# Kernel tuning notes

Hardware: AMD Instinct MI355X
Metric: run time of the kernel (lower is better)

The kernel has to match this reference:

```python
import jax, jax.numpy as jnp
import numpy as np

NUM_SEQS = 4
SEQ_LEN = 2048
T = NUM_SEQS * SEQ_LEN          # total tokens
D_IN = 4096
D_OUT = 4096
NUM_ADAPTERS = 8
MAX_RANK = 64
CACHE_LEN = NUM_ADAPTERS * MAX_RANK  # 512 pages


def setup_inputs() -> dict:
    key = jax.random.key(0)
    ks = jax.random.split(key, 8)
    x = jax.random.normal(ks[0], (T, D_IN), dtype=jnp.float32)
    weight = jax.random.normal(ks[1], (D_OUT, D_IN), dtype=jnp.float32) * 0.02
    bias = jax.random.normal(ks[2], (D_OUT,), dtype=jnp.float32) * 0.02
    a_cache = jax.random.normal(ks[3], (CACHE_LEN, D_IN), dtype=jnp.float32) * 0.02
    b_cache = jax.random.normal(ks[4], (CACHE_LEN, D_OUT), dtype=jnp.float32) * 0.02
    b_start_loc = (jnp.arange(NUM_SEQS) * SEQ_LEN).astype(jnp.int32)
    b_adapter_ids = jax.random.randint(ks[5], (NUM_SEQS,), 0, NUM_ADAPTERS).astype(jnp.int32)
    b_scaling = jax.random.uniform(ks[6], (NUM_SEQS,), dtype=jnp.float32, minval=0.5, maxval=2.0)
    # page i for (adapter a, rank slot r) lives at a*MAX_RANK + r
    rank_page_table = jnp.arange(CACHE_LEN, dtype=jnp.int32).reshape(NUM_ADAPTERS, MAX_RANK)
    ranks = jax.random.randint(ks[7], (NUM_ADAPTERS,), 1, MAX_RANK + 1).astype(jnp.int32)
    return {"x": x, "weight": weight, "bias": bias, "a_cache": a_cache,
            "b_cache": b_cache, "b_start_loc": b_start_loc,
            "b_adapter_ids": b_adapter_ids, "b_scaling": b_scaling,
            "rank_page_table": rank_page_table, "ranks": ranks}


def reference(x, weight, bias, a_cache, b_cache, b_start_loc,
              b_adapter_ids, b_scaling, rank_page_table, ranks):
    t = x.shape[0]
    num_adapters, max_rank = rank_page_table.shape
    # map each token to its sequence -> adapter id / scaling (mbgmm dispatch)
    seg = jnp.searchsorted(b_start_loc, jnp.arange(t, dtype=b_start_loc.dtype),
                           side='right') - 1                      # [T]
    tok_adapter = b_adapter_ids[seg]                              # [T]
    tok_scale = b_scaling[seg]                                    # [T]
    # gather paged LoRA A/B weights per adapter: [A, R, D]
    A_all = a_cache[rank_page_table]                              # [A, R, D_in]
    B_all = b_cache[rank_page_table]                              # [A, R, D_out]
    # mbgmm_a: xa[t, r] = x[t] . A[adapter(t), r], zero beyond rank
    xa_all = jnp.einsum('td,ard->tar', x, A_all)                  # [T, A, R]
    rmask = (jnp.arange(max_rank)[None, :] < ranks[:, None])      # [A, R]
    onehot = (tok_adapter[:, None] == jnp.arange(num_adapters)[None, :])  # [T, A]
    sel = (onehot[:, :, None] & rmask[None, :, :]).astype(x.dtype)  # [T, A, R]
    xa_sel = xa_all * sel
    # mbgmm_b: lora_out[t] = scaling * sum_r xa[t, r] * B[adapter(t), r]
    lora_out = jnp.einsum('tar,aro->to', xa_sel, B_all) * tok_scale[:, None]
    base_out = x @ weight.T + bias
    return base_out + lora_out
```

## Files before the change

### kernel.cpp

```cpp
#include <hip/hip_runtime.h>
#include <hip/hip_bf16.h>

typedef unsigned short u16;
typedef unsigned int u32;
typedef __attribute__((ext_vector_type(8))) short bf16x8;
typedef __attribute__((ext_vector_type(4))) float f32x4;

#define T_TOK 8192
#define DIN 4096
#define DOUT 4096
#define N_SEQS 4
#define N_ADPT 8
#define MAXR 64
#define CACHE_LEN 512

__device__ __forceinline__ u16 f2bf(float f) {
    u32 u = __builtin_bit_cast(u32, f);
    u += 0x7fffu + ((u >> 16) & 1u);
    return (u16)(u >> 16);
}

__device__ __forceinline__ void load_lds16(const u16* g, u16* l) {
    __builtin_amdgcn_global_load_lds(
        (const __attribute__((address_space(1))) u32*)g,
        (__attribute__((address_space(3))) u32*)l, 16, 0, 0);
}

__global__ void cvt_kernel(const float* __restrict__ in, u16* __restrict__ out, int n4) {
    int i = blockIdx.x * blockDim.x + threadIdx.x;
    int stride = gridDim.x * blockDim.x;
    for (; i < n4; i += stride) {
        float4 v = reinterpret_cast<const float4*>(in)[i];
        ushort4 o;
        o.x = f2bf(v.x); o.y = f2bf(v.y); o.z = f2bf(v.z); o.w = f2bf(v.w);
        reinterpret_cast<ushort4*>(out)[i] = o;
    }
}

__global__ void build_bt(const float* __restrict__ b_cache, const int* __restrict__ rpt,
                         u16* __restrict__ Bt) {
    int id = blockIdx.x * 256 + threadIdx.x;
    int n  = id & (DOUT - 1);
    int rb = (id >> 12) & 7;
    int a  = id >> 15;
    union { u16 u[8]; uint4 v; } pack;
    #pragma unroll
    for (int j = 0; j < 8; ++j) {
        int r = rb * 8 + j;
        int page = rpt[a * MAXR + r];
        pack.u[j] = f2bf(b_cache[(long)page * DOUT + n]);
    }
    *reinterpret_cast<uint4*>(&Bt[((long)(a * DOUT + n)) * MAXR + rb * 8]) = pack.v;
}

__launch_bounds__(256)
__global__ void xa_kernel(const u16* __restrict__ xb, const u16* __restrict__ ab,
                          const int* __restrict__ b_start_loc,
                          const int* __restrict__ b_adapter_ids,
                          const float* __restrict__ b_scaling,
                          const int* __restrict__ rpt,
                          const int* __restrict__ ranks,
                          u16* __restrict__ xa) {
    int t0 = blockIdx.x * 128;
    int seg = 0;
    #pragma unroll
    for (int i = 1; i < N_SEQS; ++i) if (b_start_loc[i] <= t0) seg = i;
    int adapter = b_adapter_ids[seg];
    float scale = b_scaling[seg];
    int rank = ranks[adapter];

    __shared__ __attribute__((aligned(16))) u16 As[128 * 32];
    __shared__ __attribute__((aligned(16))) u16 Bs[64 * 32];

    int tid = threadIdx.x;
    int lane = tid & 63, wave = tid >> 6;
    int lr = lane & 15, lk = lane >> 4;

    int e0 = wave * 64 + lane;
    int e1 = 256 + e0;
    int ra0 = e0 >> 2, ca0 = (e0 & 3) * 8;
    int ra1 = e1 >> 2, ca1 = (e1 & 3) * 8;
    const u16* gA0 = xb + (long)(t0 + ra0) * DIN + ca0;
    const u16* gA1 = xb + (long)(t0 + ra1) * DIN + ca1;
    int rB = ra0;
    int page = rpt[adapter * MAXR + rB];
    const u16* gB = ab + (long)page * DIN + ca0;

    f32x4 acc[2][4] = {};

    for (int k0 = 0; k0 < DIN; k0 += 32) {
        load_lds16(gA0 + k0, As + wave * 512);
        load_lds16(gA1 + k0, As + 2048 + wave * 512);
        load_lds16(gB + k0,  Bs + wave * 512);
        asm volatile("s_waitcnt vmcnt(0)" ::: "memory");
        __syncthreads();
        bf16x8 af[2], bfr[4];
        #pragma unroll
        for (int m = 0; m < 2; ++m)
            af[m] = *(const bf16x8*)&As[(wave * 32 + m * 16 + lr) * 32 + lk * 8];
        #pragma unroll
        for (int n = 0; n < 4; ++n)
            bfr[n] = *(const bf16x8*)&Bs[(n * 16 + lr) * 32 + lk * 8];
        #pragma unroll
        for (int m = 0; m < 2; ++m)
            #pragma unroll
            for (int n = 0; n < 4; ++n)
                acc[m][n] = __builtin_amdgcn_mfma_f32_16x16x32_bf16(af[m], bfr[n], acc[m][n], 0, 0, 0);
        __syncthreads();
    }

    #pragma unroll
    for (int m = 0; m < 2; ++m) {
        int trow = t0 + wave * 32 + m * 16 + lk * 4;
        #pragma unroll
        for (int n = 0; n < 4; ++n) {
            int r = n * 16 + lr;
            #pragma unroll
            for (int j = 0; j < 4; ++j) {
                float v = (r < rank) ? acc[m][n][j] * scale : 0.0f;
                xa[(long)(trow + j) * MAXR + r] = f2bf(v);
            }
        }
    }
}

__launch_bounds__(512, 2)
__global__ void gemm256_kernel(const u16* __restrict__ xb, const u16* __restrict__ wb,
                               const float* __restrict__ bias,
                               const u16* __restrict__ xa, const u16* __restrict__ Bt,
                               const int* __restrict__ b_start_loc,
                               const int* __restrict__ b_adapter_ids,
                               float* __restrict__ out) {
    __shared__ __attribute__((aligned(16))) u16 lds[65536];

    int bid = blockIdx.x;
    int wgid = (bid & 7) * 64 + (bid >> 3);
    int mt = wgid >> 4, nt = wgid & 15;
    int brow = mt * 256, bcol = nt * 256;

    int seg = 0;
    #pragma unroll
    for (int i = 1; i < N_SEQS; ++i) if (b_start_loc[i] <= brow) seg = i;
    int adapter = b_adapter_ids[seg];

    int tid = threadIdx.x;
    int lane = tid & 63, wave = tid >> 6;
    int wm = wave >> 2, wn = wave & 3;
    int lr = lane & 15, lk = lane >> 4;

    int rb = tid >> 3;
    int cs = (tid & 7) ^ (rb & 7);
    const u16* aSrc  = xb + (long)(brow + rb) * DIN + cs * 8;
    const u16* wSrc  = wb + (long)(bcol + rb) * DIN + cs * 8;
    const u16* xaSrc = xa + (long)(brow + rb) * MAXR + cs * 8;
    const u16* btSrc = Bt + ((long)(adapter * DOUT + bcol + rb)) * MAXR + cs * 8;

    f32x4 acc[8][4] = {};

    #define STAGE(srcA, ldA, srcB, ldB, buf)                                        \
        do {                                                                        \
            u16* al = lds + (buf) * 16384 + wave * 512;                             \
            u16* bl = lds + 32768 + (buf) * 16384 + wave * 512;                     \
            _Pragma("unroll")                                                       \
            for (int q = 0; q < 4; ++q) {                                           \
                load_lds16((srcA) + (long)(q * 64) * (ldA), al + q * 4096);         \
                load_lds16((srcB) + (long)(q * 64) * (ldB), bl + q * 4096);         \
            }                                                                       \
        } while (0)

    STAGE(aSrc, DIN, wSrc, DIN, 0);

    for (int t = 0; t <= 64; ++t) {
        int cur = t & 1;
        if (t < 63) {
            STAGE(aSrc + (t + 1) * 64, DIN, wSrc + (t + 1) * 64, DIN, cur ^ 1);
            asm volatile("s_waitcnt vmcnt(8)" ::: "memory");
        } else if (t == 63) {
            STAGE(xaSrc, MAXR, btSrc, MAXR, cur ^ 1);
            asm volatile("s_waitcnt vmcnt(8)" ::: "memory");
        } else {
            asm volatile("s_waitcnt vmcnt(0)" ::: "memory");
        }
        __builtin_amdgcn_s_barrier();
        __builtin_amdgcn_sched_barrier(0);

        const u16* Ab = lds + cur * 16384;
        const u16* Bb = lds + 32768 + cur * 16384;

        #pragma unroll
        for (int ks = 0; ks < 2; ++ks) {
            bf16x8 bfr[4];
            #pragma unroll
            for (int ni = 0; ni < 4; ++ni) {
                int row = wn * 64 + ni * 16 + lr;
                bfr[ni] = *(const bf16x8*)&Bb[row * 64 + (((ks * 4 + lk) ^ (lr & 7)) * 8)];
            }
            #pragma unroll
            for (int mh = 0; mh < 2; ++mh) {
                bf16x8 af[4];
                #pragma unroll
                for (int mi = 0; mi < 4; ++mi) {
                    int row = wm * 128 + (mh * 4 + mi) * 16 + lr;
                    af[mi] = *(const bf16x8*)&Ab[row * 64 + (((ks * 4 + lk) ^ (lr & 7)) * 8)];
                }
                __builtin_amdgcn_s_setprio(1);
                #pragma unroll
                for (int mi = 0; mi < 4; ++mi)
                    #pragma unroll
                    for (int ni = 0; ni < 4; ++ni)
                        acc[mh * 4 + mi][ni] = __builtin_amdgcn_mfma_f32_16x16x32_bf16(
                            af[mi], bfr[ni], acc[mh * 4 + mi][ni], 0, 0, 0);
                __builtin_amdgcn_s_setprio(0);
                __builtin_amdgcn_s_barrier();
                __builtin_amdgcn_sched_barrier(0);
            }
        }
    }
    #undef STAGE

    #pragma unroll
    for (int m = 0; m < 8; ++m) {
        int orow = brow + wm * 128 + m * 16 + lk * 4;
        #pragma unroll
        for (int n = 0; n < 4; ++n) {
            int ocol = bcol + wn * 64 + n * 16 + lr;
            float bv = bias[ocol];
            #pragma unroll
            for (int j = 0; j < 4; ++j)
                out[(long)(orow + j) * DOUT + ocol] = acc[m][n][j] + bv;
        }
    }
}

extern "C" void kernel_launch(void* const* d_in, const int* in_sizes, int n_in,
                              void* d_out, int out_size, void* d_ws, size_t ws_size,
                              hipStream_t stream) {
    const float* x          = (const float*)d_in[0];
    const float* weight     = (const float*)d_in[1];
    const float* bias       = (const float*)d_in[2];
    const float* a_cache    = (const float*)d_in[3];
    const float* b_cache    = (const float*)d_in[4];
    const int*   b_start    = (const int*)d_in[5];
    const int*   b_adapter  = (const int*)d_in[6];
    const float* b_scaling  = (const float*)d_in[7];
    const int*   rpt        = (const int*)d_in[8];
    const int*   ranks      = (const int*)d_in[9];
    float* out = (float*)d_out;

    char* ws = (char*)d_ws;
    u16* xb = (u16*)ws; ws += (size_t)T_TOK * DIN * 2;
    u16* wb = (u16*)ws; ws += (size_t)DOUT * DIN * 2;
    u16* ab = (u16*)ws; ws += (size_t)CACHE_LEN * DIN * 2;
    u16* Bt = (u16*)ws; ws += (size_t)N_ADPT * DOUT * MAXR * 2;
    u16* xa = (u16*)ws; ws += (size_t)T_TOK * MAXR * 2;

    cvt_kernel<<<2048, 256, 0, stream>>>(x, xb, T_TOK * DIN / 4);
    cvt_kernel<<<2048, 256, 0, stream>>>(weight, wb, DOUT * DIN / 4);
    cvt_kernel<<<512, 256, 0, stream>>>(a_cache, ab, CACHE_LEN * DIN / 4);
    build_bt<<<(N_ADPT * 8 * DOUT) / 256, 256, 0, stream>>>(b_cache, rpt, Bt);
    xa_kernel<<<T_TOK / 128, 256, 0, stream>>>(xb, ab, b_start, b_adapter, b_scaling, rpt, ranks, xa);
    gemm256_kernel<<<(T_TOK / 256) * (DOUT / 256), 512, 0, stream>>>(xb, wb, bias, xa, Bt, b_start, b_adapter, out);
}
```

Baseline: 373.6 us.

## Split K-tile staging into half-tiles interleaved with MFMA phases

Replaces the whole-tile double-buffered prefetch with a finer pipeline that stages half K-slices (ks halves) of A and B at separate points between the four MFMA phases of each iteration. It prefetches two tiles ahead, with a new LDS layout that packs two rows per 64-element line under a new swizzle. The goal is to spread global-to-LDS traffic evenly across compute and hide more load latency. The cost is more barriers per iteration and more delicate buffer-reuse ordering, which risks race conditions if a half-buffer is overwritten while it is still being read.

```diff
diff --git a/kernel.cpp b/kernel.cpp
--- a/kernel.cpp
+++ b/kernel.cpp
@@ -148,75 +148,104 @@
     int wm = wave >> 2, wn = wave & 3;
     int lr = lane & 15, lk = lane >> 4;
 
-    int rb = tid >> 3;
-    int cs = (tid & 7) ^ (rb & 7);
-    const u16* aSrc  = xb + (long)(brow + rb) * DIN + cs * 8;
-    const u16* wSrc  = wb + (long)(bcol + rb) * DIN + cs * 8;
-    const u16* xaSrc = xa + (long)(brow + rb) * MAXR + cs * 8;
-    const u16* btSrc = Bt + ((long)(adapter * DOUT + bcol + rb)) * MAXR + cs * 8;
+    int lsw = (tid & 7) ^ ((tid >> 3) & 7);
+    int c8  = (lsw & 3) * 8;
+    int r0  = (tid >> 3) * 2 + (lsw >> 2);
+    const long odA0 = (long)(brow + r0) * DIN + c8;
+    const long odA1 = odA0 + 128L * DIN;
+    const long odB0 = (long)(bcol + r0) * DIN + c8;
+    const long odB1 = odB0 + 128L * DIN;
+    const long o6A0 = (long)(brow + r0) * MAXR + c8;
+    const long o6A1 = o6A0 + 128L * MAXR;
+    const long o6B0 = (long)(adapter * DOUT + bcol + r0) * MAXR + c8;
+    const long o6B1 = o6B0 + 128L * MAXR;
+
+    #define STAGE_HALF(T, ks, isB, buf)                                            \
+        do {                                                                       \
+            u16* d = lds + (buf) * 16384 + (ks) * 8192 + ((isB) ? 32768 : 0) + tid * 8; \
+            if ((T) < 64) {                                                        \
+                long ko = (long)((T) * 64 + (ks) * 32);                            \
+                load_lds16(((isB) ? wb + odB0 : xb + odA0) + ko, d);               \
+                load_lds16(((isB) ? wb + odB1 : xb + odA1) + ko, d + 4096);        \
+            } else {                                                               \
+                long ko = (long)((ks) * 32);                                       \
+                load_lds16(((isB) ? Bt + o6B0 : xa + o6A0) + ko, d);               \
+                load_lds16(((isB) ? Bt + o6B1 : xa + o6A1) + ko, d + 4096);        \
+            }                                                                      \
+        } while (0)
+
+    #define LOADA(mh, ks)                                                          \
+        _Pragma("unroll")                                                          \
+        for (int mi = 0; mi < 4; ++mi) {                                           \
+            int r = wm * 128 + (mh) * 64 + mi * 16 + lr;                           \
+            int srr = r >> 1;                                                      \
+            af[mi] = *(const bf16x8*)&lds[b * 16384 + (ks) * 8192 + srr * 64 +     \
+                      ((((r & 1) * 4 + lk) ^ (srr & 7)) * 8)];                     \
+        }
+    #define LOADB(ks)                                                              \
+        _Pragma("unroll")                                                          \
+        for (int ni = 0; ni < 4; ++ni) {                                           \
+            int r = wn * 64 + ni * 16 + lr;                                        \
+            int srr = r >> 1;                                                      \
+            bfr[ni] = *(const bf16x8*)&lds[32768 + b * 16384 + (ks) * 8192 + srr * 64 + \
+                      ((((r & 1) * 4 + lk) ^ (srr & 7)) * 8)];                     \
+        }
+    #define MFMA16(mh)                                                             \
+        _Pragma("unroll")                                                          \
+        for (int mi = 0; mi < 4; ++mi)                                             \
+            _Pragma("unroll")                                                      \
+            for (int ni = 0; ni < 4; ++ni)                                         \
+                acc[(mh) * 4 + mi][ni] = __builtin_amdgcn_mfma_f32_16x16x32_bf16(  \
+                    af[mi], bfr[ni], acc[(mh) * 4 + mi][ni], 0, 0, 0);
+    #define BAR() do { __builtin_amdgcn_s_barrier(); __builtin_amdgcn_sched_barrier(0); } while (0)
 
     f32x4 acc[8][4] = {};
 
-    #define STAGE(srcA, ldA, srcB, ldB, buf)                                        \
-        do {                                                                        \
-            u16* al = lds + (buf) * 16384 + wave * 512;                             \
-            u16* bl = lds + 32768 + (buf) * 16384 + wave * 512;                     \
-            _Pragma("unroll")                                                       \
-            for (int q = 0; q < 4; ++q) {                                           \
-                load_lds16((srcA) + (long)(q * 64) * (ldA), al + q * 4096);         \
-                load_lds16((srcB) + (long)(q * 64) * (ldB), bl + q * 4096);         \
-            }                                                                       \
-        } while (0)
-
-    STAGE(aSrc, DIN, wSrc, DIN, 0);
+    STAGE_HALF(0, 0, false, 0);
+    STAGE_HALF(0, 0, true,  0);
+    STAGE_HALF(0, 1, false, 0);
+    STAGE_HALF(0, 1, true,  0);
+    STAGE_HALF(1, 0, true,  1);
+    STAGE_HALF(1, 0, false, 1);
+    STAGE_HALF(1, 1, true,  1);
+    asm volatile("s_waitcnt vmcnt(6)" ::: "memory");
+    BAR();
 
     for (int t = 0; t <= 64; ++t) {
-        int cur = t & 1;
-        if (t < 63) {
-            STAGE(aSrc + (t + 1) * 64, DIN, wSrc + (t + 1) * 64, DIN, cur ^ 1);
-            asm volatile("s_waitcnt vmcnt(8)" ::: "memory");
-        } else if (t == 63) {
-            STAGE(xaSrc, MAXR, btSrc, MAXR, cur ^ 1);
-            asm volatile("s_waitcnt vmcnt(8)" ::: "memory");
-        } else {
-            asm volatile("s_waitcnt vmcnt(0)" ::: "memory");
-        }
-        __builtin_amdgcn_s_barrier();
-        __builtin_amdgcn_sched_barrier(0);
-
-        const u16* Ab = lds + cur * 16384;
-        const u16* Bb = lds + 32768 + cur * 16384;
-
-        #pragma unroll
-        for (int ks = 0; ks < 2; ++ks) {
-            bf16x8 bfr[4];
-            #pragma unroll
-            for (int ni = 0; ni < 4; ++ni) {
-                int row = wn * 64 + ni * 16 + lr;
-                bfr[ni] = *(const bf16x8*)&Bb[row * 64 + (((ks * 4 + lk) ^ (lr & 7)) * 8)];
-            }
-            #pragma unroll
-            for (int mh = 0; mh < 2; ++mh) {
-                bf16x8 af[4];
-                #pragma unroll
-                for (int mi = 0; mi < 4; ++mi) {
-                    int row = wm * 128 + (mh * 4 + mi) * 16 + lr;
-                    af[mi] = *(const bf16x8*)&Ab[row * 64 + (((ks * 4 + lk) ^ (lr & 7)) * 8)];
-                }
-                __builtin_amdgcn_s_setprio(1);
-                #pragma unroll
-                for (int mi = 0; mi < 4; ++mi)
-                    #pragma unroll
-                    for (int ni = 0; ni < 4; ++ni)
-                        acc[mh * 4 + mi][ni] = __builtin_amdgcn_mfma_f32_16x16x32_bf16(
-                            af[mi], bfr[ni], acc[mh * 4 + mi][ni], 0, 0, 0);
-                __builtin_amdgcn_s_setprio(0);
-                __builtin_amdgcn_s_barrier();
-                __builtin_amdgcn_sched_barrier(0);
-            }
-        }
-    }
-    #undef STAGE
+        const int b = t & 1;
+        const int t1c = (t + 1 > 64) ? 64 : t + 1;
+        const int t2c = (t + 2 > 64) ? 64 : t + 2;
+        bf16x8 af[4], bfr[4];
+
+        LOADB(0); LOADA(0, 0);
+        STAGE_HALF(t1c, 1, false, (t + 1) & 1);
+        BAR();
+        __builtin_amdgcn_s_setprio(1); MFMA16(0); __builtin_amdgcn_s_setprio(0);
+        BAR();
+        LOADA(1, 0);
+        STAGE_HALF(t2c, 0, true, b);
+        BAR();
+        __builtin_amdgcn_s_setprio(1); MFMA16(1); __builtin_amdgcn_s_setprio(0);
+        BAR();
+        LOADB(1); LOADA(0, 1);
+        STAGE_HALF(t2c, 0, false, b);
+        BAR();
+        __builtin_amdgcn_s_setprio(1); MFMA16(0); __builtin_amdgcn_s_setprio(0);
+        BAR();
+        LOADA(1, 1);
+        STAGE_HALF(t2c, 1, true, b);
+        BAR();
+        __builtin_amdgcn_s_setprio(1); MFMA16(1); __builtin_amdgcn_s_setprio(0);
+        asm volatile("s_waitcnt vmcnt(6)" ::: "memory");
+        BAR();
+    }
+    asm volatile("s_waitcnt vmcnt(0)" ::: "memory");
+
+    #undef STAGE_HALF
+    #undef LOADA
+    #undef LOADB
+    #undef MFMA16
+    #undef BAR
 
     #pragma unroll
     for (int m = 0; m < 8; ++m) {
```

Result: no change. 374.0 us (+0.1%).

## Halve K-tile to 32 with new swizzled LDS layout in fused GEMM

Applied to the files above, without the earlier changes.

The main GEMM loop now stages K-slices of 32 instead of 64, which halves LDS usage to 64KB and doubles the iteration count to 130. Global-to-LDS loads and the LDS read addressing use a new swizzle that packs two rows per 128-byte line, and each iteration has one barrier instead of two inner barriers. The smaller LDS footprint may allow more resident workgroups or less bank conflict. In exchange there are more loop iterations, more barriers overall and shallower prefetch per stage.

```diff
diff --git a/kernel.cpp b/kernel.cpp
--- a/kernel.cpp
+++ b/kernel.cpp
@@ -131,7 +131,7 @@
                                const int* __restrict__ b_start_loc,
                                const int* __restrict__ b_adapter_ids,
                                float* __restrict__ out) {
-    __shared__ __attribute__((aligned(16))) u16 lds[65536];
+    __shared__ __attribute__((aligned(16))) u16 lds[32768];
 
     int bid = blockIdx.x;
     int wgid = (bid & 7) * 64 + (bid >> 3);
@@ -148,72 +148,80 @@
     int wm = wave >> 2, wn = wave & 3;
     int lr = lane & 15, lk = lane >> 4;
 
-    int rb = tid >> 3;
-    int cs = (tid & 7) ^ (rb & 7);
-    const u16* aSrc  = xb + (long)(brow + rb) * DIN + cs * 8;
-    const u16* wSrc  = wb + (long)(bcol + rb) * DIN + cs * 8;
-    const u16* xaSrc = xa + (long)(brow + rb) * MAXR + cs * 8;
-    const u16* btSrc = Bt + ((long)(adapter * DOUT + bcol + rb)) * MAXR + cs * 8;
+    int lsw = (tid & 7) ^ ((tid >> 3) & 7);
+    int c8  = (lsw & 3) * 8;
+    int r0  = (tid >> 3) * 2 + (lsw >> 2);
+    const long odA0 = (long)(brow + r0) * DIN + c8;
+    const long odA1 = odA0 + 128L * DIN;
+    const long odB0 = (long)(bcol + r0) * DIN + c8;
+    const long odB1 = odB0 + 128L * DIN;
+    const long o6A0 = (long)(brow + r0) * MAXR + c8;
+    const long o6A1 = o6A0 + 128L * MAXR;
+    const long o6B0 = (long)(adapter * DOUT + bcol + r0) * MAXR + c8;
+    const long o6B1 = o6B0 + 128L * MAXR;
+
+    #define STAGE(T, buf)                                                          \
+        do {                                                                       \
+            u16* dA = lds + (buf) * 8192 + tid * 8;                                \
+            u16* dB = lds + 16384 + (buf) * 8192 + tid * 8;                        \
+            if ((T) < 128) {                                                       \
+                long ko = (long)(T) * 32;                                          \
+                load_lds16(xb + odA0 + ko, dA);                                    \
+                load_lds16(xb + odA1 + ko, dA + 4096);                             \
+                load_lds16(wb + odB0 + ko, dB);                                    \
+                load_lds16(wb + odB1 + ko, dB + 4096);                             \
+            } else {                                                               \
+                long ko = (long)((T) - 128) * 32;                                  \
+                load_lds16(xa + o6A0 + ko, dA);                                    \
+                load_lds16(xa + o6A1 + ko, dA + 4096);                             \
+                load_lds16(Bt + o6B0 + ko, dB);                                    \
+                load_lds16(Bt + o6B1 + ko, dB + 4096);                             \
+            }                                                                      \
+        } while (0)
+
+    const int laneByte = (lr >> 1) * 128 + 16 * ((((lr & 1) << 2) + lk) ^ (lr >> 1));
+    const char* ldsc = (const char*)lds;
+    const int cA = wm * 8192 + laneByte;
+    const int cB = 32768 + wn * 4096 + laneByte;
 
     f32x4 acc[8][4] = {};
 
-    #define STAGE(srcA, ldA, srcB, ldB, buf)                                        \
-        do {                                                                        \
-            u16* al = lds + (buf) * 16384 + wave * 512;                             \
-            u16* bl = lds + 32768 + (buf) * 16384 + wave * 512;                     \
-            _Pragma("unroll")                                                       \
-            for (int q = 0; q < 4; ++q) {                                           \
-                load_lds16((srcA) + (long)(q * 64) * (ldA), al + q * 4096);         \
-                load_lds16((srcB) + (long)(q * 64) * (ldB), bl + q * 4096);         \
-            }                                                                       \
-        } while (0)
-
-    STAGE(aSrc, DIN, wSrc, DIN, 0);
-
-    for (int t = 0; t <= 64; ++t) {
-        int cur = t & 1;
-        if (t < 63) {
-            STAGE(aSrc + (t + 1) * 64, DIN, wSrc + (t + 1) * 64, DIN, cur ^ 1);
-            asm volatile("s_waitcnt vmcnt(8)" ::: "memory");
-        } else if (t == 63) {
-            STAGE(xaSrc, MAXR, btSrc, MAXR, cur ^ 1);
-            asm volatile("s_waitcnt vmcnt(8)" ::: "memory");
+    STAGE(0, 0);
+
+    for (int t = 0; t < 130; ++t) {
+        const int b = t & 1;
+        if (t < 129) {
+            STAGE(t + 1, b ^ 1);
+            asm volatile("s_waitcnt vmcnt(4)" ::: "memory");
         } else {
             asm volatile("s_waitcnt vmcnt(0)" ::: "memory");
         }
         __builtin_amdgcn_s_barrier();
         __builtin_amdgcn_sched_barrier(0);
 
-        const u16* Ab = lds + cur * 16384;
-        const u16* Bb = lds + 32768 + cur * 16384;
-
-        #pragma unroll
-        for (int ks = 0; ks < 2; ++ks) {
-            bf16x8 bfr[4];
-            #pragma unroll
-            for (int ni = 0; ni < 4; ++ni) {
-                int row = wn * 64 + ni * 16 + lr;
-                bfr[ni] = *(const bf16x8*)&Bb[row * 64 + (((ks * 4 + lk) ^ (lr & 7)) * 8)];
-            }
-            #pragma unroll
-            for (int mh = 0; mh < 2; ++mh) {
-                bf16x8 af[4];
-                #pragma unroll
-                for (int mi = 0; mi < 4; ++mi) {
-                    int row = wm * 128 + (mh * 4 + mi) * 16 + lr;
-                    af[mi] = *(const bf16x8*)&Ab[row * 64 + (((ks * 4 + lk) ^ (lr & 7)) * 8)];
-                }
-                __builtin_amdgcn_s_setprio(1);
-                #pragma unroll
-                for (int mi = 0; mi < 4; ++mi)
-                    #pragma unroll
-                    for (int ni = 0; ni < 4; ++ni)
-                        acc[mh * 4 + mi][ni] = __builtin_amdgcn_mfma_f32_16x16x32_bf16(
-                            af[mi], bfr[ni], acc[mh * 4 + mi][ni], 0, 0, 0);
-                __builtin_amdgcn_s_setprio(0);
-                __builtin_amdgcn_s_barrier();
-                __builtin_amdgcn_sched_barrier(0);
-            }
+        const char* pA = ldsc + b * 16384 + cA;
+        const char* pB = ldsc + b * 16384 + cB;
+
+        bf16x8 bfr[4], af[8];
+        #pragma unroll
+        for (int ni = 0; ni < 4; ++ni)
+            bfr[ni] = *(const bf16x8*)(pB + ni * 1024);
+        #pragma unroll
+        for (int mi = 0; mi < 8; ++mi)
+            af[mi] = *(const bf16x8*)(pA + mi * 1024);
+
+        __builtin_amdgcn_s_setprio(1);
+        #pragma unroll
+        for (int mi = 0; mi < 8; ++mi)
+            #pragma unroll
+            for (int ni = 0; ni < 4; ++ni)
+                acc[mi][ni] = __builtin_amdgcn_mfma_f32_16x16x32_bf16(
+                    af[mi], bfr[ni], acc[mi][ni], 0, 0, 0);
+        __builtin_amdgcn_s_setprio(0);
+
+        if (t < 129) {
+            __builtin_amdgcn_s_barrier();
+            __builtin_amdgcn_sched_barrier(0);
         }
     }
     #undef STAGE
```

Result: no change. 371.5 us (-0.5%).
